# Performance work log

Hardware: AMD Instinct MI355X
Metric: run time of the kernel (lower is better)

The kernel has to match this reference:

```python
import jax, jax.numpy as jnp
import numpy as np

TOKENS, INPUT, HIDDEN, K = 8192, 1024, 16384, 32

def setup_inputs() -> dict:
    key = jax.random.key(0)
    ks = jax.random.split(key, 6)
    return {
        "x": jax.random.normal(ks[0], (TOKENS, INPUT), dtype=jnp.float32),
        "pre_encode_b": jax.random.normal(ks[1], (INPUT,), dtype=jnp.float32) * 0.1,
        "W": jax.random.normal(ks[2], (HIDDEN, INPUT), dtype=jnp.float32) * 0.01,
        "WT": jax.random.normal(ks[3], (INPUT, HIDDEN), dtype=jnp.float32) * 0.01,
        "b1": jax.random.normal(ks[4], (HIDDEN,), dtype=jnp.float32) * 0.1,
        "b2": jax.random.normal(ks[5], (INPUT,), dtype=jnp.float32) * 0.1,
        "k": K,
    }

def reference(x, pre_encode_b, W, WT, b1, b2, k):
    # encode: dense GEMM [token, hidden]
    xc = x - pre_encode_b
    preacts = jnp.matmul(xc, WT) + b1
    # topk over hidden dim
    vals, idx = jax.lax.top_k(preacts, k)          # [token, k]
    # decode: gather rows of W by topk indices, weighted sum
    Wg = W[idx]                                    # [token, k, input]
    x_hat = jnp.einsum('tk,tki->ti', vals, Wg) + b2
    return x_hat
```

## Files before the change

### kernel.cpp

```cpp
#include <hip/hip_runtime.h>
#include <hip/hip_fp16.h>

#define TOKENS 8192
#define INPUT  1024
#define HIDDEN 16384
#define KSEL   32
#define CANDCAP 96
#define TWO_E  0.012f

typedef __attribute__((ext_vector_type(8))) short bf16x8;
typedef __attribute__((ext_vector_type(4))) float f32x4;

#define GLOAD_LDS16(g, l) __builtin_amdgcn_global_load_lds(              \
    (const __attribute__((address_space(1))) void*)(const void*)(g),     \
    (__attribute__((address_space(3))) void*)(void*)(l), 16, 0, 0)

__device__ inline short f2bf(float f) {
    unsigned u = __float_as_uint(f);
    u += 0x7FFFu + ((u >> 16) & 1u);
    return (short)(u >> 16);
}

__device__ inline float keyToF(unsigned k) {
    unsigned o = (k & 0x8000u) ? (k ^ 0x8000u) : (~k & 0xFFFFu);
    return __half2float(__ushort_as_half((unsigned short)o));
}

__global__ __launch_bounds__(256) void conv_x(
    const float* __restrict__ x, const float* __restrict__ peb,
    short* __restrict__ Abf)
{
    const int g = (blockIdx.x * 256 + threadIdx.x) * 8;
    const int col = g & (INPUT - 1);
    float4 v0 = *(const float4*)&x[g];
    float4 v1 = *(const float4*)&x[g + 4];
    float4 p0 = *(const float4*)&peb[col];
    float4 p1 = *(const float4*)&peb[col + 4];
    short o[8] = {f2bf(v0.x - p0.x), f2bf(v0.y - p0.y), f2bf(v0.z - p0.z), f2bf(v0.w - p0.w),
                  f2bf(v1.x - p1.x), f2bf(v1.y - p1.y), f2bf(v1.z - p1.z), f2bf(v1.w - p1.w)};
    *(bf16x8*)&Abf[g] = *(bf16x8*)o;
}

__global__ __launch_bounds__(256) void transp2(
    const float* __restrict__ WT, float* __restrict__ WTT, short* __restrict__ Btb)
{
    __shared__ float tl[64][65];
    const int bx = blockIdx.x, by = blockIdx.y;
    const int tid = threadIdx.x;
    const int r0 = tid >> 6, c = tid & 63;
#pragma unroll
    for (int i = 0; i < 16; ++i) {
        int r = i * 4 + r0;
        tl[r][c] = WT[(size_t)(by * 64 + r) * HIDDEN + bx * 64 + c];
    }
    __syncthreads();
#pragma unroll
    for (int i = 0; i < 16; ++i) {
        int a = i * 4 + r0;
        float v = tl[c][a];
        size_t o = (size_t)(bx * 64 + a) * INPUT + by * 64 + c;
        WTT[o] = v;
        Btb[o] = f2bf(v);
    }
}

__global__ __launch_bounds__(256) void conv_whf(
    const float* __restrict__ W, unsigned short* __restrict__ Whf)
{
    const size_t g = ((size_t)blockIdx.x * 256 + threadIdx.x) * 8;
    float4 v0 = *(const float4*)&W[g];
    float4 v1 = *(const float4*)&W[g + 4];
    unsigned short o[8] = {
        __half_as_ushort(__float2half(v0.x)), __half_as_ushort(__float2half(v0.y)),
        __half_as_ushort(__float2half(v0.z)), __half_as_ushort(__float2half(v0.w)),
        __half_as_ushort(__float2half(v1.x)), __half_as_ushort(__float2half(v1.y)),
        __half_as_ushort(__float2half(v1.z)), __half_as_ushort(__float2half(v1.w))};
    *(uint4*)&Whf[g] = *(uint4*)o;
}

__global__ __launch_bounds__(512, 2) void gemm_bf16_256(
    const short* __restrict__ A,
    const short* __restrict__ Bt,
    const float* __restrict__ bias1,
    unsigned short* __restrict__ pre16,
    int tok0)
{
    __shared__ short lds[65536];
    const char* L = (const char*)lds;
    const int tid = threadIdx.x;
    const int lane = tid & 63;
    const int w = tid >> 6;
    const int wr = w >> 2, wc = w & 3;

    const int nbx = gridDim.x;
    const int My  = gridDim.y;
    int flat = blockIdx.y * nbx + blockIdx.x;
    const int xcd = flat & 7;
    const int idx = flat >> 3;
    const int colsPerX = nbx >> 3;
    const int q = idx / My;
    const int bm = idx - q * My;
    const int bn = xcd * colsPerX + q;

    const int row0 = tok0 + bm * 256;
    const int col0 = bn * 256;

    const int xr = (lane & 7) << 4;
    const int koff = (lane >> 4) * 16;
    const int swk0 = koff ^ xr;
    const int swk1 = (64 + koff) ^ xr;
    const int aA0 = (wr * 128 + (lane & 15)) * 128 + swk0;
    const int aA1 = (wr * 128 + (lane & 15)) * 128 + swk1;
    const int aB0 = (wc * 64 + (lane & 15)) * 128 + swk0;
    const int aB1 = (wc * 64 + (lane & 15)) * 128 + swk1;

    const int srd = tid >> 3;
    const int scol = ((tid & 7) * 16) ^ ((srd & 7) << 4);
    const short* Asrc = A  + (size_t)(row0 + srd) * INPUT + (scol >> 1);
    const short* Bsrc = Bt + (size_t)(col0 + srd) * INPUT + (scol >> 1);

    f32x4 acc[8][4];
#pragma unroll
    for (int m = 0; m < 8; ++m)
#pragma unroll
        for (int n = 0; n < 4; ++n) acc[m][n] = (f32x4){0.f, 0.f, 0.f, 0.f};

    auto stageA = [&](int slot, int half, int kt) {
        const size_t so = (size_t)(half * 128) * INPUT + kt * 64;
        short* dst = lds + slot * 32768 + half * 8192 + tid * 8;
        GLOAD_LDS16(Asrc + so, dst);
        GLOAD_LDS16(Asrc + so + (size_t)64 * INPUT, dst + 4096);
    };
    auto stageB = [&](int slot, int half, int kt) {
        const size_t so = (size_t)(half * 128) * INPUT + kt * 64;
        short* dst = lds + slot * 32768 + 16384 + half * 8192 + tid * 8;
        GLOAD_LDS16(Bsrc + so, dst);
        GLOAD_LDS16(Bsrc + so + (size_t)64 * INPUT, dst + 4096);
    };

    bf16x8 AQ[8], BL[4], BH[4];

#define RD_A(SAb, mfbase)                                                       \
    _Pragma("unroll") for (int mf = 0; mf < 4; ++mf) {                          \
        AQ[mf * 2 + 0] = *(const bf16x8*)(L + (SAb) + aA0 + ((mfbase) + mf) * 2048); \
        AQ[mf * 2 + 1] = *(const bf16x8*)(L + (SAb) + aA1 + ((mfbase) + mf) * 2048); \
    }
#define RD_B(SBb, BF, nfbase)                                                   \
    _Pragma("unroll") for (int nf = 0; nf < 2; ++nf) {                          \
        BF[nf * 2 + 0] = *(const bf16x8*)(L + (SBb) + aB0 + ((nfbase) + nf) * 2048); \
        BF[nf * 2 + 1] = *(const bf16x8*)(L + (SBb) + aB1 + ((nfbase) + nf) * 2048); \
    }
#define MFMA_Q(BF, mb, nb)                                                      \
    __builtin_amdgcn_s_setprio(1);                                              \
    _Pragma("unroll") for (int mf = 0; mf < 4; ++mf)                            \
        _Pragma("unroll") for (int nf = 0; nf < 2; ++nf)                        \
            _Pragma("unroll") for (int kk = 0; kk < 2; ++kk)                    \
                acc[(mb) + mf][(nb) + nf] = __builtin_amdgcn_mfma_f32_16x16x32_bf16( \
                    AQ[mf * 2 + kk], BF[nf * 2 + kk], acc[(mb) + mf][(nb) + nf], 0, 0, 0); \
    __builtin_amdgcn_s_setprio(0);
#define BAR()  __builtin_amdgcn_s_barrier()
#define LGKM0() asm volatile("s_waitcnt lgkmcnt(0)" ::: "memory")

    stageA(0, 0, 0); stageA(0, 1, 0);
    stageB(0, 0, 0); stageB(0, 1, 0);
    stageB(1, 0, 1); stageB(1, 1, 1);
    asm volatile("s_waitcnt vmcnt(4)" ::: "memory");
    BAR();

    for (int i = 0; i < 8; ++i) {
        const int kt1 = 2 * i + 1, kt2 = 2 * i + 2, kt3 = 2 * i + 3;
        const bool s2 = kt2 < 16, s3 = kt3 < 16;
        RD_A(0, 0); RD_B(32768, BL, 0);
        stageA(1, 0, kt1);
        BAR(); LGKM0();
        MFMA_Q(BL, 0, 0);
        BAR();
        RD_B(32768, BH, 2);
        stageA(1, 1, kt1);
        BAR(); LGKM0();
        MFMA_Q(BH, 0, 2);
        BAR();
        RD_A(0, 4);
        if (s2) stageB(0, 0, kt2);
        BAR(); LGKM0();
        MFMA_Q(BL, 4, 0);
        BAR();
        if (s2) stageB(0, 1, kt2);
        BAR(); LGKM0();
        MFMA_Q(BH, 4, 2);
        if (i < 7) { asm volatile("s_waitcnt vmcnt(4)" ::: "memory"); }
        else       { asm volatile("s_waitcnt vmcnt(0)" ::: "memory"); }
        BAR();
        RD_A(65536, 0); RD_B(98304, BL, 0);
        if (s2) stageA(0, 0, kt2);
        BAR(); LGKM0();
        MFMA_Q(BL, 0, 0);
        BAR();
        RD_B(98304, BH, 2);
        if (s2) stageA(0, 1, kt2);
        BAR(); LGKM0();
        MFMA_Q(BH, 0, 2);
        BAR();
        RD_A(65536, 4);
        if (s3) stageB(1, 0, kt3);
        BAR(); LGKM0();
        MFMA_Q(BL, 4, 0);
        BAR();
        if (s3) stageB(1, 1, kt3);
        BAR(); LGKM0();
        MFMA_Q(BH, 4, 2);
        if (i < 7) { asm volatile("s_waitcnt vmcnt(4)" ::: "memory"); }
        BAR();
    }
#undef RD_A
#undef RD_B
#undef MFMA_Q
#undef BAR
#undef LGKM0

    __syncthreads();

    float bb[4];
#pragma unroll
    for (int nf = 0; nf < 4; ++nf)
        bb[nf] = bias1[col0 + wc * 64 + nf * 16 + (lane & 15)];

    unsigned short* LE = (unsigned short*)lds;
#pragma unroll
    for (int mf = 0; mf < 8; ++mf) {
#pragma unroll
        for (int nf = 0; nf < 4; ++nf) {
#pragma unroll
            for (int r = 0; r < 4; ++r) {
                int er = wr * 16 + (lane >> 4) * 4 + r;
                int ec = wc * 64 + nf * 16 + (lane & 15);
                LE[er * 264 + ec] = __half_as_ushort(__float2half(acc[mf][nf][r] + bb[nf]));
            }
        }
        __syncthreads();
#pragma unroll
        for (int rd = 0; rd < 2; ++rd) {
            int idx2 = rd * 512 + tid;
            int er = idx2 >> 5, c8 = (idx2 & 31) * 8;
            int b = er >> 4;
            int grow = bm * 256 + b * 128 + mf * 16 + (er & 15);
            uint4 v = *(const uint4*)&LE[er * 264 + c8];
            *(uint4*)&pre16[(size_t)grow * HIDDEN + col0 + c8] = v;
        }
        __syncthreads();
    }
}

__global__ __launch_bounds__(256) void topcand3(
    const unsigned short* __restrict__ pre16,
    int* __restrict__ cand, float* __restrict__ scr,
    int* __restrict__ ncand, int tok0)
{
    const int tid = threadIdx.x;
    const int t = blockIdx.x;
    const unsigned short* row = pre16 + (size_t)t * HIDDEN;

    unsigned pk[32];
#pragma unroll
    for (int i = 0; i < 8; ++i) {
        uint4 raw = *(const uint4*)&row[(size_t)tid * 64 + i * 8];
        unsigned rr[4] = {raw.x, raw.y, raw.z, raw.w};
#pragma unroll
        for (int j = 0; j < 4; ++j) {
            unsigned lo16 = rr[j] & 0xFFFFu, hi16 = rr[j] >> 16;
            lo16 ^= (((lo16 >> 15) * 0xFFFFu) | 0x8000u);
            hi16 ^= (((hi16 >> 15) * 0xFFFFu) | 0x8000u);
            pk[i * 4 + j] = lo16 | (hi16 << 16);
        }
    }

    __shared__ unsigned wsum[4];
    const int lane = tid & 63, wid = tid >> 6;

    auto countGE = [&](unsigned tau) -> unsigned {
        unsigned c = 0;
#pragma unroll
        for (int i = 0; i < 32; ++i) {
            c += ((pk[i] & 0xFFFFu) >= tau) ? 1u : 0u;
            c += ((pk[i] >> 16) >= tau) ? 1u : 0u;
        }
#pragma unroll
        for (int s = 32; s > 0; s >>= 1) c += __shfl_xor(c, s, 64);
        if (lane == 0) wsum[wid] = c;
        __syncthreads();
        unsigned tot = wsum[0] + wsum[1] + wsum[2] + wsum[3];
        __syncthreads();
        return tot;
    };

    unsigned lo = 0, hi = 0xFFFFu;
    for (int it = 0; it < 17 && lo < hi; ++it) {
        unsigned mid = (lo + hi + 1) >> 1;
        unsigned c = countGE(mid);
        if (c >= 40u) { lo = mid; if (c <= 48u) break; }
        else hi = mid - 1;
    }
    float v40 = keyToF(lo);
    float vthr = v40 - (TWO_E + 0.002f);
    unsigned kthr = (unsigned)__half_as_ushort(__float2half(vthr));
    kthr ^= (((kthr >> 15) * 0xFFFFu) | 0x8000u);

    unsigned mycnt = 0;
#pragma unroll
    for (int i = 0; i < 32; ++i) {
        mycnt += ((pk[i] & 0xFFFFu) >= kthr) ? 1u : 0u;
        mycnt += ((pk[i] >> 16) >= kthr) ? 1u : 0u;
    }
    unsigned inc = mycnt;
#pragma unroll
    for (int s = 1; s < 64; s <<= 1) {
        unsigned o = __shfl_up(inc, s, 64);
        if (lane >= s) inc += o;
    }
    __shared__ unsigned wtot[4];
    if (lane == 63) wtot[wid] = inc;
    __syncthreads();
    unsigned base = inc - mycnt;
    for (int k = 0; k < wid; ++k) base += wtot[k];
    unsigned tot = wtot[0] + wtot[1] + wtot[2] + wtot[3];

    const int gtok = tok0 + t;
    unsigned pos = base;
#pragma unroll
    for (int i = 0; i < 32; ++i) {
        unsigned l16 = pk[i] & 0xFFFFu, h16 = pk[i] >> 16;
        if (l16 >= kthr) {
            if (pos < CANDCAP) {
                cand[(size_t)gtok * CANDCAP + pos] = tid * 64 + i * 2;
                scr[(size_t)gtok * CANDCAP + pos] = keyToF(l16);
            }
            ++pos;
        }
        if (h16 >= kthr) {
            if (pos < CANDCAP) {
                cand[(size_t)gtok * CANDCAP + pos] = tid * 64 + i * 2 + 1;
                scr[(size_t)gtok * CANDCAP + pos] = keyToF(h16);
            }
            ++pos;
        }
    }
    if (tid == 0) ncand[gtok] = (int)(tot < (unsigned)CANDCAP ? tot : (unsigned)CANDCAP);
}

__global__ __launch_bounds__(256) void rescore_band_decode(
    const float* __restrict__ x, const float* __restrict__ peb,
    const float* __restrict__ WTT, const float* __restrict__ bias1,
    const int* __restrict__ cand, const float* __restrict__ scr,
    const int* __restrict__ ncand,
    const unsigned short* __restrict__ Whf, const float* __restrict__ b2,
    float* __restrict__ out)
{
    const int t = blockIdx.x;
    const int tid = threadIdx.x;
    __shared__ double xcs[INPUT];
    __shared__ float sv[CANDCAP];
    __shared__ int   si[CANDCAP];
    __shared__ double bex[CANDCAP];
    __shared__ unsigned char flg[CANDCAP];
    __shared__ unsigned char self_[CANDCAP];
    __shared__ short bandlist[CANDCAP];
    __shared__ float s32s;
    __shared__ int bns, nins;
    __shared__ float sel_v[KSEL];
    __shared__ int sel_i[KSEL];

    const int nc0 = ncand[t];
    const int nc = nc0 < CANDCAP ? nc0 : CANDCAP;

#pragma unroll
    for (int i = 0; i < 4; ++i) {
        int j = tid + i * 256;
        xcs[j] = (double)x[(size_t)t * INPUT + j] - (double)peb[j];
    }
    if (tid < nc) {
        sv[tid] = scr[(size_t)t * CANDCAP + tid];
        si[tid] = cand[(size_t)t * CANDCAP + tid];
    }
    __syncthreads();

    if (tid < nc) {
        float v = sv[tid]; int h = si[tid];
        int r = 0;
        for (int k = 0; k < nc; ++k) {
            float vk = sv[k];
            if (vk > v || (vk == v && si[k] < h)) ++r;
        }
        if (r == 31) s32s = v;
    }
    __syncthreads();
    const float s32 = s32s;

    if (tid < nc) {
        float v = sv[tid];
        flg[tid] = (v > s32 + TWO_E) ? 2 : ((v >= s32 - TWO_E) ? 1 : 0);
    }
    __syncthreads();
    if (tid == 0) {
        int bn = 0, nin = 0;
        for (int k = 0; k < nc; ++k) {
            if (flg[k] == 1) bandlist[bn++] = (short)k;
            else if (flg[k] == 2) ++nin;
        }
        bns = bn; nins = nin;
    }
    __syncthreads();
    const int bn = bns, need = KSEL - nins;

    const int wid = tid >> 6, lane = tid & 63;
    for (int j0 = wid * 2; j0 < bn; j0 += 8) {
        const int j1 = j0 + 1;
        const int c0 = bandlist[j0];
        const int c1 = (j1 < bn) ? bandlist[j1] : c0;
        const int h0 = si[c0], h1 = si[c1];
        const float* w0 = WTT + (size_t)h0 * INPUT;
        const float* w1 = WTT + (size_t)h1 * INPUT;
        double s0 = 0.0, s1 = 0.0;
#pragma unroll
        for (int st = 0; st < 16; ++st) {
            const double xv = xcs[lane + st * 64];
            s0 += (double)w0[lane + st * 64] * xv;
            s1 += (double)w1[lane + st * 64] * xv;
        }
#pragma unroll
        for (int off = 32; off > 0; off >>= 1) {
            s0 += __shfl_xor(s0, off, 64);
            s1 += __shfl_xor(s1, off, 64);
        }
        if (lane == 0) {
            bex[c0] = s0 + (double)bias1[h0];
            if (j1 < bn) bex[c1] = s1 + (double)bias1[h1];
        }
    }
    __syncthreads();

    if (tid < nc) {
        int s = 0;
        if (flg[tid] == 2) s = 1;
        else if (flg[tid] == 1) {
            double v = bex[tid]; int h = si[tid];
            int r = 0;
            for (int k = 0; k < bn; ++k) {
                int ck = bandlist[k];
                double vk = bex[ck];
                if (vk > v || (vk == v && si[ck] < h)) ++r;
            }
            if (r < need) s = 1;
        }
        self_[tid] = (unsigned char)s;
    }
    __syncthreads();
    if (tid < nc && self_[tid]) {
        int pos = 0;
        for (int k = 0; k < tid; ++k) pos += self_[k];
        if (pos < KSEL) {
            sel_v[pos] = (flg[tid] == 2) ? sv[tid] : (float)bex[tid];
            sel_i[pos] = si[tid];
        }
    }
    __syncthreads();

    const int c = tid * 4;
    float4 acc = *(const float4*)&b2[c];
#pragma unroll 8
    for (int j = 0; j < KSEL; ++j) {
        const int h = sel_i[j];
        uint2 raw = *(const uint2*)&Whf[(size_t)h * INPUT + c];
        const float s = sel_v[j];
        __half2 p0 = *(__half2*)&raw.x;
        __half2 p1 = *(__half2*)&raw.y;
        float2 f0 = __half22float2(p0);
        float2 f1 = __half22float2(p1);
        acc.x += s * f0.x; acc.y += s * f0.y; acc.z += s * f1.x; acc.w += s * f1.y;
    }
    *(float4*)&out[(size_t)t * INPUT + c] = acc;
}

extern "C" void kernel_launch(void* const* d_in, const int* in_sizes, int n_in,
                              void* d_out, int out_size, void* d_ws, size_t ws_size,
                              hipStream_t stream) {
    const float* x   = (const float*)d_in[0];
    const float* peb = (const float*)d_in[1];
    const float* W   = (const float*)d_in[2];
    const float* WT  = (const float*)d_in[3];
    const float* b1  = (const float*)d_in[4];
    const float* b2  = (const float*)d_in[5];
    float* out = (float*)d_out;

    char* p = (char*)d_ws;
    int*   candb = (int*)p;            p += (size_t)TOKENS * CANDCAP * 4;
    float* scrb  = (float*)p;          p += (size_t)TOKENS * CANDCAP * 4;
    int*   ncb   = (int*)p;            p += (size_t)TOKENS * 4;
    float* WTT   = (float*)p;          p += (size_t)HIDDEN * INPUT * 4;
    short* Abf   = (short*)p;          p += (size_t)TOKENS * INPUT * 2;
    short* Btb   = (short*)p;          p += (size_t)HIDDEN * INPUT * 2;
    unsigned short* Whf = (unsigned short*)p; p += (size_t)HIDDEN * INPUT * 2;
    unsigned short* pre16 = (unsigned short*)p;

    size_t used = (size_t)(p - (char*)d_ws);
    size_t avail = ws_size > used ? ws_size - used : 0;
    long cap = (long)(avail / ((size_t)HIDDEN * 2));
    cap = (cap / 256) * 256;
    if (cap > 2048) cap = 2048;
    if (cap < 256) cap = 256;

    conv_x<<<dim3(TOKENS * INPUT / (256 * 8)), dim3(256), 0, stream>>>(x, peb, Abf);
    transp2<<<dim3(HIDDEN / 64, INPUT / 64), dim3(256), 0, stream>>>(WT, WTT, Btb);
    conv_whf<<<dim3((unsigned)((size_t)HIDDEN * INPUT / (256 * 8))), dim3(256), 0, stream>>>(W, Whf);

    for (int tok0 = 0; tok0 < TOKENS; tok0 += (int)cap) {
        int M = TOKENS - tok0;
        if (M > cap) M = (int)cap;
        gemm_bf16_256<<<dim3(HIDDEN / 256, M / 256), dim3(512), 0, stream>>>(
            Abf, Btb, b1, pre16, tok0);
        topcand3<<<dim3(M), dim3(256), 0, stream>>>(pre16, candb, scrb, ncb, tok0);
    }

    rescore_band_decode<<<dim3(TOKENS), dim3(256), 0, stream>>>(
        x, peb, WTT, b1, candb, scrb, ncb, Whf, b2, out);
}
```

Before: 691.7 us.

## Split rescore and decode into separate kernels and narrow the rescore band

Splits the fused rescore-and-decode kernel in two. The first kernel writes the selected top-k values and indices to a global buffer. A new 512-thread decode kernel splits the 32 gathered rows across two halves and reduces them through shared memory, to expose more memory-level parallelism in the gather. It also halves the TWO_E band threshold so fewer candidates need exact fp64 rescoring, which risks misordering near-tied candidates and adds an extra launch plus a global round-trip.

```diff
diff --git a/kernel.cpp b/kernel.cpp
--- a/kernel.cpp
+++ b/kernel.cpp
@@ -6,7 +6,7 @@
 #define HIDDEN 16384
 #define KSEL   32
 #define CANDCAP 96
-#define TWO_E  0.012f
+#define TWO_E  0.006f
 
 typedef __attribute__((ext_vector_type(8))) short bf16x8;
 typedef __attribute__((ext_vector_type(4))) float f32x4;
@@ -347,13 +347,12 @@
     if (tid == 0) ncand[gtok] = (int)(tot < (unsigned)CANDCAP ? tot : (unsigned)CANDCAP);
 }
 
-__global__ __launch_bounds__(256) void rescore_band_decode(
+__global__ __launch_bounds__(256) void rescore_select(
     const float* __restrict__ x, const float* __restrict__ peb,
     const float* __restrict__ WTT, const float* __restrict__ bias1,
     const int* __restrict__ cand, const float* __restrict__ scr,
     const int* __restrict__ ncand,
-    const unsigned short* __restrict__ Whf, const float* __restrict__ b2,
-    float* __restrict__ out)
+    float* __restrict__ selv, int* __restrict__ seli)
 {
     const int t = blockIdx.x;
     const int tid = threadIdx.x;
@@ -366,8 +365,6 @@
     __shared__ short bandlist[CANDCAP];
     __shared__ float s32s;
     __shared__ int bns, nins;
-    __shared__ float sel_v[KSEL];
-    __shared__ int sel_i[KSEL];
 
     const int nc0 = ncand[t];
     const int nc = nc0 < CANDCAP ? nc0 : CANDCAP;
@@ -458,26 +455,49 @@
         int pos = 0;
         for (int k = 0; k < tid; ++k) pos += self_[k];
         if (pos < KSEL) {
-            sel_v[pos] = (flg[tid] == 2) ? sv[tid] : (float)bex[tid];
-            sel_i[pos] = si[tid];
-        }
-    }
-    __syncthreads();
-
-    const int c = tid * 4;
-    float4 acc = *(const float4*)&b2[c];
+            selv[(size_t)t * KSEL + pos] = (flg[tid] == 2) ? sv[tid] : (float)bex[tid];
+            seli[(size_t)t * KSEL + pos] = si[tid];
+        }
+    }
+}
+
+__global__ __launch_bounds__(512) void decode512(
+    const float* __restrict__ selv, const int* __restrict__ seli,
+    const unsigned short* __restrict__ Whf, const float* __restrict__ b2,
+    float* __restrict__ out)
+{
+    const int t = blockIdx.x;
+    const int tid = threadIdx.x;
+    const int jh = tid >> 8;
+    const int cpos = tid & 255;
+    const int c = cpos * 4;
+    __shared__ float sv[KSEL];
+    __shared__ int si[KSEL];
+    __shared__ float4 red[256];
+    if (tid < KSEL) {
+        sv[tid] = selv[(size_t)t * KSEL + tid];
+        si[tid] = seli[(size_t)t * KSEL + tid];
+    }
+    __syncthreads();
+    float4 acc = {0.f, 0.f, 0.f, 0.f};
+    const int j0 = jh * 16;
 #pragma unroll 8
-    for (int j = 0; j < KSEL; ++j) {
-        const int h = sel_i[j];
-        uint2 raw = *(const uint2*)&Whf[(size_t)h * INPUT + c];
-        const float s = sel_v[j];
-        __half2 p0 = *(__half2*)&raw.x;
-        __half2 p1 = *(__half2*)&raw.y;
-        float2 f0 = __half22float2(p0);
-        float2 f1 = __half22float2(p1);
+    for (int j = j0; j < j0 + 16; ++j) {
+        uint2 raw = *(const uint2*)&Whf[(size_t)si[j] * INPUT + c];
+        const float s = sv[j];
+        float2 f0 = __half22float2(*(__half2*)&raw.x);
+        float2 f1 = __half22float2(*(__half2*)&raw.y);
         acc.x += s * f0.x; acc.y += s * f0.y; acc.z += s * f1.x; acc.w += s * f1.y;
     }
-    *(float4*)&out[(size_t)t * INPUT + c] = acc;
+    if (jh == 1) red[cpos] = acc;
+    __syncthreads();
+    if (jh == 0) {
+        float4 o = red[cpos];
+        float4 bb = *(const float4*)&b2[c];
+        o.x += acc.x + bb.x; o.y += acc.y + bb.y;
+        o.z += acc.z + bb.z; o.w += acc.w + bb.w;
+        *(float4*)&out[(size_t)t * INPUT + c] = o;
+    }
 }
 
 extern "C" void kernel_launch(void* const* d_in, const int* in_sizes, int n_in,
@@ -495,6 +515,8 @@
     int*   candb = (int*)p;            p += (size_t)TOKENS * CANDCAP * 4;
     float* scrb  = (float*)p;          p += (size_t)TOKENS * CANDCAP * 4;
     int*   ncb   = (int*)p;            p += (size_t)TOKENS * 4;
+    float* selvb = (float*)p;          p += (size_t)TOKENS * KSEL * 4;
+    int*   selib = (int*)p;            p += (size_t)TOKENS * KSEL * 4;
     float* WTT   = (float*)p;          p += (size_t)HIDDEN * INPUT * 4;
     short* Abf   = (short*)p;          p += (size_t)TOKENS * INPUT * 2;
     short* Btb   = (short*)p;          p += (size_t)HIDDEN * INPUT * 2;
@@ -520,6 +542,7 @@
         topcand3<<<dim3(M), dim3(256), 0, stream>>>(pre16, candb, scrb, ncb, tok0);
     }
 
-    rescore_band_decode<<<dim3(TOKENS), dim3(256), 0, stream>>>(
-        x, peb, WTT, b1, candb, scrb, ncb, Whf, b2, out);
-}
+    rescore_select<<<dim3(TOKENS), dim3(256), 0, stream>>>(
+        x, peb, WTT, b1, candb, scrb, ncb, selvb, selib);
+    decode512<<<dim3(TOKENS), dim3(512), 0, stream>>>(selvb, selib, Whf, b2, out);
+}
```

Result: no change. 698.3 us (+1.0%).
